# Kernel optimization log

Hardware: AMD Instinct MI355X
Metric: run time of the kernel (lower is better)

## Reference

```python
import jax, jax.numpy as jnp
import numpy as np

B, N, D = 2, 2048, 1024
H = 16
DH = D // H

def setup_inputs() -> dict:
    key = jax.random.key(0)
    ks = jax.random.split(key, 9)
    s = 1.0 / np.sqrt(D)
    return {
        "x": jax.random.normal(ks[0], (B, N, D), dtype=jnp.float32),
        "Wq": jax.random.uniform(ks[1], (D, D), jnp.float32, -s, s),
        "bq": jax.random.uniform(ks[2], (D,), jnp.float32, -s, s),
        "Wk": jax.random.uniform(ks[3], (D, D), jnp.float32, -s, s),
        "bk": jax.random.uniform(ks[4], (D,), jnp.float32, -s, s),
        "Wv": jax.random.uniform(ks[5], (D, D), jnp.float32, -s, s),
        "bv": jax.random.uniform(ks[6], (D,), jnp.float32, -s, s),
        "Wo": jax.random.uniform(ks[7], (D, D), jnp.float32, -s, s),
        "bo": jax.random.uniform(ks[8], (D,), jnp.float32, -s, s),
    }

def reference(x, Wq, bq, Wk, bk, Wv, bv, Wo, bo):
    # torch Linear: y = x @ W.T + b
    scale = 1.0 / np.sqrt(DH)
    q = (x @ Wq.T + bq).reshape(B, N, H, DH).transpose(0, 2, 1, 3)  # [B,H,N,DH]
    k = (x @ Wk.T + bk).reshape(B, N, H, DH).transpose(0, 2, 1, 3)
    v = (x @ Wv.T + bv).reshape(B, N, H, DH).transpose(0, 2, 1, 3)
    scores = jnp.einsum('bhnd,bhmd->bhnm', q, k) * scale  # [B,H,N,N]
    attn = jax.nn.softmax(scores, axis=-1)
    out = jnp.einsum('bhnm,bhmd->bhnd', attn, v)  # [B,H,N,DH]
    out = out.transpose(0, 2, 1, 3).reshape(B, N, D)
    return out @ Wo.T + bo
```

## Files before the change

kernel.cpp:

```cpp
#include <hip/hip_runtime.h>
#include <hip/hip_bf16.h>

#define B_  2
#define N_  2048
#define D_  1024
#define H_  16
#define DH_ 64
#define BN_ (B_*N_)

typedef __attribute__((ext_vector_type(8))) short short8;
typedef __attribute__((ext_vector_type(4))) float f32x4;
typedef __attribute__((ext_vector_type(16))) float f32x16;
typedef __attribute__((ext_vector_type(4))) unsigned int uint4v;

typedef __attribute__((address_space(3))) unsigned int lds_u32_t;
typedef const __attribute__((address_space(1))) unsigned int glb_u32_t;

__device__ __forceinline__ void async_load16(const unsigned short* g, unsigned short* l) {
    __builtin_amdgcn_global_load_lds((glb_u32_t*)g, (lds_u32_t*)l, 16, 0, 0);
}

__device__ __forceinline__ unsigned short f2bf(float f) {
    __hip_bfloat16 h = __float2bfloat16(f);
    return *reinterpret_cast<unsigned short*>(&h);
}

__device__ __forceinline__ unsigned int pkbf(float a, float b) {
    unsigned int ua = __float_as_uint(a) + 0x8000u;
    unsigned int ub = __float_as_uint(b) + 0x8000u;
    return __builtin_amdgcn_perm(ub, ua, 0x07060302);
}

#if __has_builtin(__builtin_amdgcn_exp2f)
#define EXP2(x) __builtin_amdgcn_exp2f(x)
#else
#define EXP2(x) exp2f(x)
#endif

#define QSCL 0.1803368801111204f

__global__ __launch_bounds__(256) void cast_kernel(
    const float* __restrict__ x,  const float* __restrict__ wq,
    const float* __restrict__ wk, const float* __restrict__ wv,
    const float* __restrict__ wo,
    unsigned short* __restrict__ xb,  unsigned short* __restrict__ wqb,
    unsigned short* __restrict__ wkb, unsigned short* __restrict__ wvb,
    unsigned short* __restrict__ wob)
{
    const size_t NX = (size_t)BN_ * D_;
    const size_t NW = (size_t)D_ * D_;
    size_t i = ((size_t)blockIdx.x * 256 + threadIdx.x) * 4;
    const float* src; unsigned short* dst; size_t off;
    if (i < NX) { src = x; dst = xb; off = i; }
    else {
        size_t j = (i - NX) >> 20;
        off = (i - NX) & (NW - 1);
        src = (j == 0) ? wq : (j == 1) ? wk : (j == 2) ? wv : wo;
        dst = (j == 0) ? wqb : (j == 1) ? wkb : (j == 2) ? wvb : wob;
    }
    float4 v = *(const float4*)(src + off);
    ushort4 o;
    o.x = f2bf(v.x); o.y = f2bf(v.y); o.z = f2bf(v.z); o.w = f2bf(v.w);
    *(ushort4*)(dst + off) = o;
}

template<int OUT_MODE>
__device__ __forceinline__ void gemm_body(
    unsigned short* __restrict__ As, unsigned short* __restrict__ Bs,
    const unsigned short* __restrict__ A, const unsigned short* __restrict__ W,
    const float* __restrict__ bias, void* __restrict__ Cout, int bx, int by)
{
    constexpr int K = D_;
    const int tid  = threadIdx.x;
    const int lane = tid & 63;
    const int wave = tid >> 6;
    const int wm = wave & 1, wn = wave >> 1;
    const int l15 = lane & 15, quad = lane >> 4;

    f32x4 acc[4][4] = {};
    const int row0 = by * 128, col0 = bx * 128;

    const int srow = lane >> 3;
    const int scb  = lane & 7;

    for (int k0 = 0; k0 < K; k0 += 64) {
        __syncthreads();
#pragma unroll
        for (int cc = 0; cc < 4; ++cc) {
            int c  = wave * 4 + cc;
            int lr = c * 8 + srow;
            int gcol = k0 + ((scb ^ (lr & 7)) * 8);
            async_load16(A + (size_t)(row0 + lr) * K + gcol, As + c * 512);
            async_load16(W + (size_t)(col0 + lr) * K + gcol, Bs + c * 512);
        }
        __syncthreads();

#pragma unroll
        for (int kf = 0; kf < 2; ++kf) {
            const int swz = ((kf * 4 + quad) ^ (l15 & 7)) * 8;
            short8 af[4], bf[4];
#pragma unroll
            for (int mi = 0; mi < 4; mi++)
                af[mi] = *(const short8*)(&As[(wm * 64 + mi * 16 + l15) * 64 + swz]);
#pragma unroll
            for (int ni = 0; ni < 4; ni++)
                bf[ni] = *(const short8*)(&Bs[(wn * 64 + ni * 16 + l15) * 64 + swz]);
#pragma unroll
            for (int mi = 0; mi < 4; mi++)
#pragma unroll
                for (int ni = 0; ni < 4; ni++)
                    acc[mi][ni] = __builtin_amdgcn_mfma_f32_16x16x32_bf16(
                        af[mi], bf[ni], acc[mi][ni], 0, 0, 0);
        }
    }

#pragma unroll
    for (int ni = 0; ni < 4; ni++) {
        int col = col0 + wn * 64 + ni * 16 + l15;
        float bv = bias[col];
#pragma unroll
        for (int mi = 0; mi < 4; mi++) {
            int row = row0 + wm * 64 + mi * 16 + quad * 4;
            if (OUT_MODE == 2) {
                ushort4 pk;
                pk.x = f2bf(acc[mi][ni][0] + bv);
                pk.y = f2bf(acc[mi][ni][1] + bv);
                pk.z = f2bf(acc[mi][ni][2] + bv);
                pk.w = f2bf(acc[mi][ni][3] + bv);
                *(ushort4*)((unsigned short*)Cout + (size_t)col * BN_ + row) = pk;
            } else {
#pragma unroll
                for (int r = 0; r < 4; r++) {
                    float v = acc[mi][ni][r] + bv;
                    if (OUT_MODE == 3) v *= QSCL;
                    if (OUT_MODE == 0)
                        ((float*)Cout)[(size_t)(row + r) * D_ + col] = v;
                    else
                        ((unsigned short*)Cout)[(size_t)(row + r) * D_ + col] = f2bf(v);
                }
            }
        }
    }
}

__global__ __launch_bounds__(256) void qkv_gemm(
    const unsigned short* __restrict__ xb,
    const unsigned short* __restrict__ wqb, const unsigned short* __restrict__ wkb,
    const unsigned short* __restrict__ wvb,
    const float* __restrict__ bq, const float* __restrict__ bk, const float* __restrict__ bv,
    unsigned short* __restrict__ q, unsigned short* __restrict__ k, unsigned short* __restrict__ vt)
{
    __shared__ __align__(16) unsigned short As[128 * 64];
    __shared__ __align__(16) unsigned short Bs[128 * 64];
    if (blockIdx.z == 0)
        gemm_body<3>(As, Bs, xb, wqb, bq, q,  blockIdx.x, blockIdx.y);
    else if (blockIdx.z == 1)
        gemm_body<1>(As, Bs, xb, wkb, bk, k,  blockIdx.x, blockIdx.y);
    else
        gemm_body<2>(As, Bs, xb, wvb, bv, vt, blockIdx.x, blockIdx.y);
}

__global__ __launch_bounds__(256) void out_gemm(
    const unsigned short* __restrict__ attn, const unsigned short* __restrict__ wob,
    const float* __restrict__ bo, float* __restrict__ out)
{
    __shared__ __align__(16) unsigned short As[128 * 64];
    __shared__ __align__(16) unsigned short Bs[128 * 64];
    gemm_body<0>(As, Bs, attn, wob, bo, out, blockIdx.x, blockIdx.y);
}

__global__ __launch_bounds__(256, 4) void attn_split(
    const unsigned short* __restrict__ q, const unsigned short* __restrict__ k,
    const unsigned short* __restrict__ vt,
    float* __restrict__ opart, float* __restrict__ lspart)
{
    __shared__ __align__(16) unsigned short Ks[2][64 * 64];
    __shared__ __align__(16) unsigned short Vs[2][64 * 64];

    const int tid = threadIdx.x;
    const int lane = tid & 63, wave = tid >> 6;
    const int l31 = lane & 31, kq = lane >> 5;
    const int bh = blockIdx.x;
    const int qt = blockIdx.y;
    const int z  = blockIdx.z;
    const int b = bh >> 4, h = bh & 15;

    const unsigned short* qb = q  + (size_t)b * N_ * D_ + h * DH_;
    const unsigned short* kb = k  + (size_t)b * N_ * D_ + h * DH_;
    const unsigned short* vb = vt + (size_t)h * DH_ * BN_ + (size_t)b * N_;

    const int qrow0 = qt * 128 + wave * 32;
    const int kvbase = z * (N_ / 2);

    short8 qf[4];
#pragma unroll
    for (int s = 0; s < 4; s++)
        qf[s] = *(const short8*)(qb + (size_t)(qrow0 + l31) * D_ + s * 16 + kq * 8);

    f32x16 oacc[2] = {};
    float lsum = 0.f;

    const int srow = lane >> 3, scb = lane & 7;

    auto stage = [&](int bi, int kv0) {
#pragma unroll
        for (int cc = 0; cc < 2; ++cc) {
            int c  = wave * 2 + cc;
            int lr = c * 8 + srow;
            int swz8 = (scb ^ (lr & 7)) * 8;
            async_load16(kb + (size_t)(kv0 + lr) * D_ + swz8, (unsigned short*)Ks[bi] + c * 512);
            async_load16(vb + (size_t)lr * BN_ + kv0 + swz8,  (unsigned short*)Vs[bi] + c * 512);
        }
    };

    stage(0, kvbase);

    const int NIT = (N_ / 2) / 64;
    for (int it = 0; it < NIT; ++it) {
        const int cur = it & 1;
        __syncthreads();
        if (it + 1 < NIT) stage(cur ^ 1, kvbase + (it + 1) * 64);

        const unsigned short* Kc = Ks[cur];
        const unsigned short* Vc = Vs[cur];

#pragma unroll
        for (int mb = 0; mb < 2; mb++) {
            f32x16 st = {};
#pragma unroll
            for (int s = 0; s < 4; s++) {
                short8 kfr = *(const short8*)((const char*)Kc +
                    (mb * 32 + l31) * 128 + (((2 * s + kq) ^ (l31 & 7)) * 16));
                st = __builtin_amdgcn_mfma_f32_32x32x16_bf16(kfr, qf[s], st, 0, 0, 0);
            }

            unsigned int pk[8];
#pragma unroll
            for (int g = 0; g < 4; g++) {
                float p0 = EXP2(st[g * 4 + 0]);
                float p1 = EXP2(st[g * 4 + 1]);
                float p2 = EXP2(st[g * 4 + 2]);
                float p3 = EXP2(st[g * 4 + 3]);
                lsum += (p0 + p1) + (p2 + p3);
                pk[2 * g + 0] = pkbf(p0, p1);
                pk[2 * g + 1] = pkbf(p2, p3);
            }
#pragma unroll
            for (int s = 0; s < 2; s++) {
                uint4v fu;
                fu[0] = pk[4 * s + 0]; fu[1] = pk[4 * s + 1];
                fu[2] = pk[4 * s + 2]; fu[3] = pk[4 * s + 3];
                short8 pf = __builtin_bit_cast(short8, fu);
                const int blkA = 4 * mb + 2 * s;
#pragma unroll
                for (int nb = 0; nb < 2; nb++) {
                    const char* vrow = (const char*)Vc + (nb * 32 + l31) * 128;
                    uint2 vlo = *(const uint2*)(vrow + ((blkA       ^ (l31 & 7)) * 16) + kq * 8);
                    uint2 vhi = *(const uint2*)(vrow + (((blkA + 1) ^ (l31 & 7)) * 16) + kq * 8);
                    uint4v vu; vu[0] = vlo.x; vu[1] = vlo.y; vu[2] = vhi.x; vu[3] = vhi.y;
                    short8 vf = __builtin_bit_cast(short8, vu);
                    oacc[nb] = __builtin_amdgcn_mfma_f32_32x32x16_bf16(
                        pf, vf, oacc[nb], 0, 0, 0);
                }
            }
        }
    }

    lsum += __shfl_xor(lsum, 32);
    if (kq == 0)
        lspart[(size_t)z * (32 * 2048) + ((size_t)bh << 11) + qrow0 + l31] = lsum;

    float* op = opart + (size_t)z * ((size_t)BN_ * D_);
#pragma unroll
    for (int g = 0; g < 4; g++)
#pragma unroll
        for (int rr = 0; rr < 4; rr++) {
            int reg = g * 4 + rr;
            int row = qrow0 + rr + 8 * g + 4 * kq;
            size_t base = ((size_t)b * N_ + row) * D_ + h * DH_;
#pragma unroll
            for (int nb = 0; nb < 2; nb++)
                op[base + nb * 32 + l31] = oacc[nb][reg];
        }
}

__global__ __launch_bounds__(256) void combine_kernel(
    const float* __restrict__ opart, const float* __restrict__ lspart,
    unsigned short* __restrict__ ad)
{
    const size_t HALF = (size_t)BN_ * D_;
    size_t i = ((size_t)blockIdx.x * 256 + threadIdx.x) * 4;
    int bn = (int)(i >> 10);
    int h  = (int)((i >> 6) & 15);
    int b  = bn >> 11, n = bn & 2047;
    float4 a = *(const float4*)(opart + i);
    float4 c = *(const float4*)(opart + HALF + i);
    size_t li = (((size_t)(b * 16 + h)) << 11) + n;
    float l = lspart[li] + lspart[li + 32 * 2048];
    float inv = 1.f / l;
    ushort4 r;
    r.x = f2bf((a.x + c.x) * inv);
    r.y = f2bf((a.y + c.y) * inv);
    r.z = f2bf((a.z + c.z) * inv);
    r.w = f2bf((a.w + c.w) * inv);
    *(ushort4*)(ad + i) = r;
}

__global__ __launch_bounds__(256) void attn_kernel(
    const unsigned short* __restrict__ q, const unsigned short* __restrict__ k,
    const unsigned short* __restrict__ vt, unsigned short* __restrict__ o)
{
    __shared__ __align__(16) unsigned short Ks[2][64 * 64];
    __shared__ __align__(16) unsigned short Vs[2][64 * 64];

    const int tid = threadIdx.x;
    const int lane = tid & 63, wave = tid >> 6;
    const int l31 = lane & 31, kq = lane >> 5;
    const int bh = blockIdx.x;
    const int qt = blockIdx.y;
    const int b = bh >> 4, h = bh & 15;

    const unsigned short* qb = q  + (size_t)b * N_ * D_ + h * DH_;
    const unsigned short* kb = k  + (size_t)b * N_ * D_ + h * DH_;
    const unsigned short* vb = vt + (size_t)h * DH_ * BN_ + (size_t)b * N_;

    const int qrow0 = qt * 128 + wave * 32;

    short8 qf[4];
#pragma unroll
    for (int s = 0; s < 4; s++)
        qf[s] = *(const short8*)(qb + (size_t)(qrow0 + l31) * D_ + s * 16 + kq * 8);

    f32x16 oacc[2] = {};
    float lsum = 0.f;

    const int srow = lane >> 3, scb = lane & 7;

    auto stage = [&](int bi, int kv0) {
#pragma unroll
        for (int cc = 0; cc < 2; ++cc) {
            int c  = wave * 2 + cc;
            int lr = c * 8 + srow;
            int swz8 = (scb ^ (lr & 7)) * 8;
            async_load16(kb + (size_t)(kv0 + lr) * D_ + swz8, (unsigned short*)Ks[bi] + c * 512);
            async_load16(vb + (size_t)lr * BN_ + kv0 + swz8,  (unsigned short*)Vs[bi] + c * 512);
        }
    };

    stage(0, 0);

    const int NIT = N_ / 64;
    for (int it = 0; it < NIT; ++it) {
        const int cur = it & 1;
        __syncthreads();
        if (it + 1 < NIT) stage(cur ^ 1, (it + 1) * 64);

        const unsigned short* Kc = Ks[cur];
        const unsigned short* Vc = Vs[cur];

        f32x16 st[2] = {};
#pragma unroll
        for (int s = 0; s < 4; s++) {
#pragma unroll
            for (int mb = 0; mb < 2; mb++) {
                short8 kfr = *(const short8*)((const char*)Kc +
                    (mb * 32 + l31) * 128 + (((2 * s + kq) ^ (l31 & 7)) * 16));
                st[mb] = __builtin_amdgcn_mfma_f32_32x32x16_bf16(
                    kfr, qf[s], st[mb], 0, 0, 0);
            }
        }

#pragma unroll
        for (int mb = 0; mb < 2; mb++) {
            unsigned int pk[8];
#pragma unroll
            for (int g = 0; g < 4; g++) {
                float p0 = EXP2(st[mb][g * 4 + 0]);
                float p1 = EXP2(st[mb][g * 4 + 1]);
                float p2 = EXP2(st[mb][g * 4 + 2]);
                float p3 = EXP2(st[mb][g * 4 + 3]);
                lsum += (p0 + p1) + (p2 + p3);
                pk[2 * g + 0] = pkbf(p0, p1);
                pk[2 * g + 1] = pkbf(p2, p3);
            }
#pragma unroll
            for (int s = 0; s < 2; s++) {
                uint4v fu;
                fu[0] = pk[4 * s + 0]; fu[1] = pk[4 * s + 1];
                fu[2] = pk[4 * s + 2]; fu[3] = pk[4 * s + 3];
                short8 pf = __builtin_bit_cast(short8, fu);
                const int blkA = 4 * mb + 2 * s;
#pragma unroll
                for (int nb = 0; nb < 2; nb++) {
                    const char* vrow = (const char*)Vc + (nb * 32 + l31) * 128;
                    uint2 vlo = *(const uint2*)(vrow + ((blkA       ^ (l31 & 7)) * 16) + kq * 8);
                    uint2 vhi = *(const uint2*)(vrow + (((blkA + 1) ^ (l31 & 7)) * 16) + kq * 8);
                    uint4v vu; vu[0] = vlo.x; vu[1] = vlo.y; vu[2] = vhi.x; vu[3] = vhi.y;
                    short8 vf = __builtin_bit_cast(short8, vu);
                    oacc[nb] = __builtin_amdgcn_mfma_f32_32x32x16_bf16(
                        pf, vf, oacc[nb], 0, 0, 0);
                }
            }
        }
    }

    lsum += __shfl_xor(lsum, 32);
    __syncthreads();
    float* Lt = (float*)&Ks[0][0] + wave * 32;
    if (kq == 0) Lt[l31] = lsum;
    asm volatile("s_waitcnt lgkmcnt(0)" ::: "memory");

#pragma unroll
    for (int g = 0; g < 4; g++)
#pragma unroll
        for (int rr = 0; rr < 4; rr++) {
            int reg = g * 4 + rr;
            float inv = 1.f / Lt[rr + 8 * g + 4 * kq];
            int row = qrow0 + rr + 8 * g + 4 * kq;
            size_t base = ((size_t)b * N_ + row) * D_ + h * DH_;
#pragma unroll
            for (int nb = 0; nb < 2; nb++)
                o[base + nb * 32 + l31] = f2bf(oacc[nb][reg] * inv);
        }
}

extern "C" void kernel_launch(void* const* d_in, const int* in_sizes, int n_in,
                              void* d_out, int out_size, void* d_ws, size_t ws_size,
                              hipStream_t stream)
{
    const float* x  = (const float*)d_in[0];
    const float* Wq = (const float*)d_in[1];
    const float* bq = (const float*)d_in[2];
    const float* Wk = (const float*)d_in[3];
    const float* bk = (const float*)d_in[4];
    const float* Wv = (const float*)d_in[5];
    const float* bv = (const float*)d_in[6];
    const float* Wo = (const float*)d_in[7];
    const float* bo = (const float*)d_in[8];
    float* out = (float*)d_out;

    char* ws = (char*)d_ws;
    unsigned short* xb  = (unsigned short*)(ws + 0);
    unsigned short* wqb = (unsigned short*)(ws + 8388608);
    unsigned short* wkb = (unsigned short*)(ws + 10485760);
    unsigned short* wvb = (unsigned short*)(ws + 12582912);
    unsigned short* wob = (unsigned short*)(ws + 14680064);
    unsigned short* qd  = (unsigned short*)(ws + 16777216);
    unsigned short* kd  = (unsigned short*)(ws + 25165824);
    unsigned short* vtd = (unsigned short*)(ws + 33554432);
    unsigned short* ad  = (unsigned short*)(ws + 41943040);
    float* opart = (float*)(ws + 50331648);
    float* lsw   = (float*)(ws + 83886080);
    const size_t WS_NEED_SPLIT = 84410368;

    cast_kernel<<<8192, 256, 0, stream>>>(x, Wq, Wk, Wv, Wo, xb, wqb, wkb, wvb, wob);
    qkv_gemm<<<dim3(8, 32, 3), 256, 0, stream>>>(xb, wqb, wkb, wvb, bq, bk, bv, qd, kd, vtd);
    if (ws_size >= WS_NEED_SPLIT) {
        attn_split<<<dim3(32, 16, 2), 256, 0, stream>>>(qd, kd, vtd, opart, lsw);
        combine_kernel<<<4096, 256, 0, stream>>>(opart, lsw, ad);
    } else {
        attn_kernel<<<dim3(32, 16), 256, 0, stream>>>(qd, kd, vtd, ad);
    }
    out_gemm<<<dim3(8, 32), 256, 0, stream>>>(ad, wob, bo, out);
}
```

Measured before the change: 215.3 us.

## Add four-way KV split for attention and XCD-aware block swizzle in GEMMs

Templates the split-KV attention and combine kernels on the number of splits and launches a four-way split when the workspace is large enough, falling back to two-way or unsplit otherwise. The four-way split doubles the attention grid to fill more compute units, but doubles the fp32 partial-output traffic written by attention and read back by the combine pass. It also remaps GEMM block indices so that consecutive blocks dispatched to the same XCD cover neighbouring output tiles, aiming for better L2 reuse.

```diff
diff --git a/kernel.cpp b/kernel.cpp
--- a/kernel.cpp
+++ b/kernel.cpp
@@ -143,6 +143,12 @@
     }
 }
 
+__device__ __forceinline__ void xcd_swz(int& bx, int& by) {
+    int w = blockIdx.y * 8 + blockIdx.x;
+    int s = (w & 7) * 32 + (w >> 3);
+    bx = s & 7; by = s >> 3;
+}
+
 __global__ __launch_bounds__(256) void qkv_gemm(
     const unsigned short* __restrict__ xb,
     const unsigned short* __restrict__ wqb, const unsigned short* __restrict__ wkb,
@@ -152,12 +158,13 @@
 {
     __shared__ __align__(16) unsigned short As[128 * 64];
     __shared__ __align__(16) unsigned short Bs[128 * 64];
+    int bx, by; xcd_swz(bx, by);
     if (blockIdx.z == 0)
-        gemm_body<3>(As, Bs, xb, wqb, bq, q,  blockIdx.x, blockIdx.y);
+        gemm_body<3>(As, Bs, xb, wqb, bq, q,  bx, by);
     else if (blockIdx.z == 1)
-        gemm_body<1>(As, Bs, xb, wkb, bk, k,  blockIdx.x, blockIdx.y);
+        gemm_body<1>(As, Bs, xb, wkb, bk, k,  bx, by);
     else
-        gemm_body<2>(As, Bs, xb, wvb, bv, vt, blockIdx.x, blockIdx.y);
+        gemm_body<2>(As, Bs, xb, wvb, bv, vt, bx, by);
 }
 
 __global__ __launch_bounds__(256) void out_gemm(
@@ -166,9 +173,11 @@
 {
     __shared__ __align__(16) unsigned short As[128 * 64];
     __shared__ __align__(16) unsigned short Bs[128 * 64];
-    gemm_body<0>(As, Bs, attn, wob, bo, out, blockIdx.x, blockIdx.y);
-}
-
+    int bx, by; xcd_swz(bx, by);
+    gemm_body<0>(As, Bs, attn, wob, bo, out, bx, by);
+}
+
+template<int NS>
 __global__ __launch_bounds__(256, 4) void attn_split(
     const unsigned short* __restrict__ q, const unsigned short* __restrict__ k,
     const unsigned short* __restrict__ vt,
@@ -190,7 +199,7 @@
     const unsigned short* vb = vt + (size_t)h * DH_ * BN_ + (size_t)b * N_;
 
     const int qrow0 = qt * 128 + wave * 32;
-    const int kvbase = z * (N_ / 2);
+    const int kvbase = z * (N_ / NS);
 
     short8 qf[4];
 #pragma unroll
@@ -215,7 +224,7 @@
 
     stage(0, kvbase);
 
-    const int NIT = (N_ / 2) / 64;
+    const int NIT = (N_ / NS) / 64;
     for (int it = 0; it < NIT; ++it) {
         const int cur = it & 1;
         __syncthreads();
@@ -284,6 +293,7 @@
         }
 }
 
+template<int NS>
 __global__ __launch_bounds__(256) void combine_kernel(
     const float* __restrict__ opart, const float* __restrict__ lspart,
     unsigned short* __restrict__ ad)
@@ -294,15 +304,24 @@
     int h  = (int)((i >> 6) & 15);
     int b  = bn >> 11, n = bn & 2047;
     float4 a = *(const float4*)(opart + i);
-    float4 c = *(const float4*)(opart + HALF + i);
-    size_t li = (((size_t)(b * 16 + h)) << 11) + n;
-    float l = lspart[li] + lspart[li + 32 * 2048];
+    float l;
+    {
+        size_t li = (((size_t)(b * 16 + h)) << 11) + n;
+        l = lspart[li];
+#pragma unroll
+        for (int z = 1; z < NS; z++) l += lspart[li + (size_t)z * (32 * 2048)];
+    }
+#pragma unroll
+    for (int z = 1; z < NS; z++) {
+        float4 c = *(const float4*)(opart + (size_t)z * HALF + i);
+        a.x += c.x; a.y += c.y; a.z += c.z; a.w += c.w;
+    }
     float inv = 1.f / l;
     ushort4 r;
-    r.x = f2bf((a.x + c.x) * inv);
-    r.y = f2bf((a.y + c.y) * inv);
-    r.z = f2bf((a.z + c.z) * inv);
-    r.w = f2bf((a.w + c.w) * inv);
+    r.x = f2bf(a.x * inv);
+    r.y = f2bf(a.y * inv);
+    r.z = f2bf(a.z * inv);
+    r.w = f2bf(a.w * inv);
     *(ushort4*)(ad + i) = r;
 }
 
@@ -450,14 +469,19 @@
     unsigned short* vtd = (unsigned short*)(ws + 33554432);
     unsigned short* ad  = (unsigned short*)(ws + 41943040);
     float* opart = (float*)(ws + 50331648);
-    float* lsw   = (float*)(ws + 83886080);
-    const size_t WS_NEED_SPLIT = 84410368;
+    float* lsw4  = (float*)(ws + 117440512);
+    float* lsw2  = (float*)(ws + 83886080);
+    const size_t WS_NEED4 = 118489088;
+    const size_t WS_NEED2 = 84410368;
 
     cast_kernel<<<8192, 256, 0, stream>>>(x, Wq, Wk, Wv, Wo, xb, wqb, wkb, wvb, wob);
     qkv_gemm<<<dim3(8, 32, 3), 256, 0, stream>>>(xb, wqb, wkb, wvb, bq, bk, bv, qd, kd, vtd);
-    if (ws_size >= WS_NEED_SPLIT) {
-        attn_split<<<dim3(32, 16, 2), 256, 0, stream>>>(qd, kd, vtd, opart, lsw);
-        combine_kernel<<<4096, 256, 0, stream>>>(opart, lsw, ad);
+    if (ws_size >= WS_NEED4) {
+        attn_split<4><<<dim3(32, 16, 4), 256, 0, stream>>>(qd, kd, vtd, opart, lsw4);
+        combine_kernel<4><<<4096, 256, 0, stream>>>(opart, lsw4, ad);
+    } else if (ws_size >= WS_NEED2) {
+        attn_split<2><<<dim3(32, 16, 2), 256, 0, stream>>>(qd, kd, vtd, opart, lsw2);
+        combine_kernel<2><<<4096, 256, 0, stream>>>(opart, lsw2, ad);
     } else {
         attn_kernel<<<dim3(32, 16), 256, 0, stream>>>(qd, kd, vtd, ad);
     }
```

Result: no change. 215.5 us (+0.1%).
